# Optimization experiments

Measured on AMD Instinct MI355X. Metric: run time of the kernel, lower is better.

The kernel has to match this reference:

```python
import jax, jax.numpy as jnp
import numpy as np

B, C, H, W = 4, 256, 32, 32
DS, DC, EXP, NSL, NH = 16, 4, 2, 16, 2
DI = EXP * C
DTR = (C + 15) // 16


def layer_norm(x, w, b, eps=1e-5):
    m = x.mean(-1, keepdims=True)
    v = ((x - m) ** 2).mean(-1, keepdims=True)
    return (x - m) / jnp.sqrt(v + eps) * w + b


def conv2d(x, w, b, groups=1, pad=1):
    y = jax.lax.conv_general_dilated(x, w, (1, 1), [(pad, pad), (pad, pad)],
        dimension_numbers=('NCHW', 'OIHW', 'NCHW'), feature_group_count=groups)
    return y + b[None, :, None, None]


def causal_conv1d(x, w, b):
    k = w.shape[-1]
    y = jax.lax.conv_general_dilated(x, w, (1,), [(k - 1, 0)],
        dimension_numbers=('NCH', 'OIH', 'NCH'), feature_group_count=x.shape[1])
    return y + b[None, :, None]


def selective_scan(u, delta, A, Bm, Cm, D, z):
    # u, delta, z: (b,d,l); A: (d,n); Bm, Cm: (b,n,l); D: (d,)
    dA = jnp.exp(jnp.einsum('bdl,dn->lbdn', delta, A))
    dBu = jnp.einsum('bdl,bnl->lbdn', delta * u, Bm)
    Cl = jnp.moveaxis(Cm, -1, 0)  # (l,b,n)
    def step(s, inp):
        dA_t, dBu_t, C_t = inp
        s = dA_t * s + dBu_t
        return s, jnp.einsum('bdn,bn->bd', s, C_t)
    s0 = jnp.zeros(dA.shape[1:], dA.dtype)
    _, ys = jax.lax.scan(step, s0, (dA, dBu, Cl))
    y = jnp.moveaxis(ys, 0, -1) + D[None, :, None] * u
    return y * jax.nn.silu(z)


def mamba_inner(xz, cw, cb, xpw, dtw, dtb, A, D):
    d = xz.shape[1] // 2
    xm, z = xz[:, :d], xz[:, d:]
    xm = jax.nn.silu(causal_conv1d(xm, cw, cb))
    x_dbl = jnp.einsum('bdl,ed->ble', xm, xpw)  # e = dt_rank + 2*d_state
    dt = x_dbl[..., :DTR]
    Bm = x_dbl[..., DTR:DTR + DS]
    Cm = x_dbl[..., DTR + DS:]
    dt = jax.nn.softplus(jnp.einsum('blr,dr->bdl', dt, dtw) + dtb[None, :, None])
    return selective_scan(xm, dt, A, jnp.moveaxis(Bm, -1, 1), jnp.moveaxis(Cm, -1, 1), D, z)


def mamba_v3(hs, in_w, cw, cb, cbw, cbb, csw, csb, xpw, xpbw, xpsw,
             dtw, dtb, dtbw, dtbb, dtsw, dtsb, Alog, Ablog, Aslog, D, Db, Ds, outw):
    b, l, dm = hs.shape
    xz = jnp.einsum('bld,ed->bel', hs, in_w)  # (b, 2*DI, l)
    A, A_b, A_s = -jnp.exp(Alog), -jnp.exp(Ablog), -jnp.exp(Aslog)
    out = mamba_inner(xz, cw, cb, xpw, dtw, dtb, A, D)
    out_b = mamba_inner(xz[:, :, ::-1], cbw, cbb, xpbw, dtbw, dtbb, A_b, Db)
    # slice scan: torch.chunk(nslices,-1) -> stack(-1) -> flatten(-2)
    xz_s = xz.reshape(b, 2 * DI, NSL, l // NSL).transpose(0, 1, 3, 2).reshape(b, 2 * DI, l)
    out_s = mamba_inner(xz_s, csw, csb, xpsw, dtsw, dtsb, A_s, Ds)
    # restore: reshape(b,d,nslices,l//nslices).permute(0,1,3,2).flatten(-2)
    out_s = out_s.reshape(b, DI, NSL, l // NSL).transpose(0, 1, 3, 2).reshape(b, DI, l)
    comb = out + out_b[:, :, ::-1] + out_s
    return jnp.einsum('bdl,od->blo', comb, outw)


def forward(x, proj1_w, proj1_b, proj2_w, proj2_b, norm_w, norm_b,
            q_w, q_b, k_w, k_b, v_w, v_b, o_w, o_b, fc1_w, fc1_b, dw_w, dw_b,
            in_w, cw, cb, cbw, cbb, csw, csb, xpw, xpbw, xpsw,
            dtw, dtb, dtbw, dtbb, dtsw, dtsb, Alog, Ablog, Aslog, D, Db, Ds, outw):
    b, c, h, w = x.shape
    n = h * w
    x_skip = x
    # torch: x.transpose(1,2).reshape(B,C,H,W) -- memory reinterpret, replicated
    x_flat = jnp.transpose(x, (0, 2, 1, 3)).reshape(b, c, h, w)
    xc = conv2d(x_flat, proj1_w, proj1_b)
    xc = jnp.transpose(xc.reshape(b, c, n), (0, 2, 1))
    xc = layer_norm(xc, norm_w, norm_b)
    dh = c // NH
    Q = (xc @ q_w.T + q_b).reshape(b, n, NH, dh).transpose(0, 2, 1, 3)
    K = (xc @ k_w.T + k_b).reshape(b, n, NH, dh).transpose(0, 2, 1, 3)
    V = (xc @ v_w.T + v_b).reshape(b, n, NH, dh).transpose(0, 2, 1, 3)
    scores = jnp.einsum('bhqd,bhkd->bhqk', Q, K) / jnp.sqrt(jnp.float32(dh))
    probs = jax.nn.softmax(scores, axis=-1)
    att = jnp.einsum('bhqk,bhkd->bhqd', probs, V).transpose(0, 2, 1, 3).reshape(b, n, c)
    att = att @ o_w.T + o_b
    # torch: .view(B,C,HW).transpose(1,2) -- memory reinterpret, replicated
    x_att = jnp.transpose(att.reshape(b, c, n), (0, 2, 1))
    xm = mamba_v3(x_att, in_w, cw, cb, cbw, cbb, csw, csb, xpw, xpbw, xpsw,
                  dtw, dtb, dtbw, dtbb, dtsw, dtsb, Alog, Ablog, Aslog, D, Db, Ds, outw)
    xm = jnp.transpose(xm, (0, 2, 1)).reshape(b, c, h, w)
    xm = jax.nn.relu(conv2d(xm, proj1_w, proj1_b))  # proj1 reused (as in source)
    xm = jax.nn.relu(conv2d(xm, proj2_w, proj2_b, pad=0))
    xs = jnp.transpose(xm.reshape(b, c, n), (0, 2, 1))
    xf = xs @ fc1_w.T + fc1_b
    xd = jnp.transpose(xf, (0, 2, 1)).reshape(b, c, h, w)
    xd = conv2d(xd, dw_w, dw_b, groups=c)
    xd = jnp.transpose(xd.reshape(b, c, n), (0, 2, 1))
    out = jnp.transpose(xd.reshape(b, h, w, c), (0, 3, 1, 2)) + x_skip
    return out


def setup_inputs():
    keys = iter(jax.random.split(jax.random.key(0), 64))
    def rn(shape, s=0.02):
        return jax.random.normal(next(keys), shape, jnp.float32) * s
    Alog = jnp.log(jnp.tile(jnp.arange(1, DS + 1, dtype=jnp.float32), (DI, 1)))
    return dict(
        x=jax.random.normal(next(keys), (B, C, H, W), jnp.float32),
        proj1_w=rn((C, C, 3, 3)), proj1_b=jnp.zeros((C,), jnp.float32),
        proj2_w=rn((C, C, 1, 1)), proj2_b=jnp.zeros((C,), jnp.float32),
        norm_w=jnp.ones((C,), jnp.float32), norm_b=jnp.zeros((C,), jnp.float32),
        q_w=rn((C, C)), q_b=jnp.zeros((C,), jnp.float32),
        k_w=rn((C, C)), k_b=jnp.zeros((C,), jnp.float32),
        v_w=rn((C, C)), v_b=jnp.zeros((C,), jnp.float32),
        o_w=rn((C, C)), o_b=jnp.zeros((C,), jnp.float32),
        fc1_w=rn((C, C)), fc1_b=jnp.zeros((C,), jnp.float32),
        dw_w=rn((C, 1, 3, 3)), dw_b=jnp.zeros((C,), jnp.float32),
        in_w=rn((2 * DI, C)),
        cw=rn((DI, 1, DC), 0.1), cb=jnp.zeros((DI,), jnp.float32),
        cbw=rn((DI, 1, DC), 0.1), cbb=jnp.zeros((DI,), jnp.float32),
        csw=rn((DI, 1, DC), 0.1), csb=jnp.zeros((DI,), jnp.float32),
        xpw=rn((DTR + 2 * DS, DI)), xpbw=rn((DTR + 2 * DS, DI)), xpsw=rn((DTR + 2 * DS, DI)),
        dtw=rn((DI, DTR), 0.1), dtb=jnp.full((DI,), -4.6, jnp.float32),
        dtbw=rn((DI, DTR), 0.1), dtbb=jnp.full((DI,), -4.6, jnp.float32),
        dtsw=rn((DI, DTR), 0.1), dtsb=jnp.full((DI,), -4.6, jnp.float32),
        Alog=Alog, Ablog=Alog, Aslog=Alog,
        D=jnp.ones((DI,), jnp.float32), Db=jnp.ones((DI,), jnp.float32), Ds=jnp.ones((DI,), jnp.float32),
        outw=rn((C, DI)),
    )


def reference(x, proj1_w, proj1_b, proj2_w, proj2_b, norm_w, norm_b,
              q_w, q_b, k_w, k_b, v_w, v_b, o_w, o_b, fc1_w, fc1_b, dw_w, dw_b,
              in_w, cw, cb, cbw, cbb, csw, csb, xpw, xpbw, xpsw,
              dtw, dtb, dtbw, dtbb, dtsw, dtsb, Alog, Ablog, Aslog, D, Db, Ds, outw):
    return forward(x, proj1_w, proj1_b, proj2_w, proj2_b, norm_w, norm_b,
                   q_w, q_b, k_w, k_b, v_w, v_b, o_w, o_b, fc1_w, fc1_b, dw_w, dw_b,
                   in_w, cw, cb, cbw, cbb, csw, csb, xpw, xpbw, xpsw,
                   dtw, dtb, dtbw, dtbb, dtsw, dtsb, Alog, Ablog, Aslog, D, Db, Ds, outw)
```

## Files before the change

kernel.cpp:

```cpp
#include <hip/hip_runtime.h>


#define LOG2E 1.4426950408889634f
#define NCH 16
#define LCH 64

typedef unsigned short u16;
typedef unsigned int u32;
typedef __attribute__((ext_vector_type(8))) short bf16x8;
typedef __attribute__((ext_vector_type(4))) float f32x4;

__device__ __forceinline__ u16 f2b(float f) {
  u32 u = __builtin_bit_cast(u32, f);
  u32 r = (u + 0x7fffu + ((u >> 16) & 1u)) >> 16;
  return (u16)r;
}
__device__ __forceinline__ float b2f(u16 h) {
  u32 u = ((u32)h) << 16;
  return __builtin_bit_cast(float, u);
}

#define DPP_ADD(p, ctrl)                                                   \
  (p) += __builtin_bit_cast(float, __builtin_amdgcn_update_dpp(            \
             0, __builtin_bit_cast(int, (p)), ctrl, 0xF, 0xF, true))

static const long BRS = 44544;

struct BrP { const float *cw, *cb, *xpw, *dtw, *dtb, *Al, *Dv; };

__global__ __launch_bounds__(256) void pack_branch_k(float* __restrict__ dst0,
                                                     BrP p0, BrP p1, BrP p2) {
  int z = blockIdx.y;
  BrP p = (z == 0) ? p0 : ((z == 1) ? p1 : p2);
  float* dst = dst0 + (long)z * BRS;
  int t = blockIdx.x * 256 + threadIdx.x;
  if (t < 2048) dst[t] = p.cw[t];
  else if (t < 2560) dst[t] = p.cb[t - 2048];
  else if (t < 27136) dst[t] = p.xpw[t - 2560];
  else if (t < 35328) dst[t] = p.dtw[t - 27136];
  else if (t < 35840) dst[t] = p.dtb[t - 35328];
  else if (t < 44032) dst[t] = -expf(p.Al[t - 35840]) * LOG2E;
  else if (t < 44544) dst[t] = p.Dv[t - 44032];
}

__global__ __launch_bounds__(256) void pack_wb_k(
    const float* __restrict__ qw, const float* __restrict__ kw,
    const float* __restrict__ vw, const float* __restrict__ ow,
    const float* __restrict__ inw, const float* __restrict__ outw,
    const float* __restrict__ p2w, const float* __restrict__ fc1w,
    const float* __restrict__ qb, const float* __restrict__ kb,
    const float* __restrict__ vb, u16* __restrict__ WB,
    float* __restrict__ QBIAS) {
  int t = blockIdx.x * 256 + threadIdx.x;
  if (t < 65536) WB[t] = f2b(qw[t]);
  else if (t < 131072) WB[t] = f2b(kw[t - 65536]);
  else if (t < 196608) WB[t] = f2b(vw[t - 131072]);
  else if (t < 262144) WB[t] = f2b(ow[t - 196608]);
  else if (t < 524288) WB[t] = f2b(inw[t - 262144]);
  else if (t < 655360) WB[t] = f2b(outw[t - 524288]);
  else if (t < 720896) WB[t] = f2b(p2w[t - 655360]);
  else if (t < 786432) WB[t] = f2b(fc1w[t - 720896]);
  else if (t < 787200) {
    int i = t - 786432;
    QBIAS[i] = (i < 256) ? qb[i] : (i < 512 ? kb[i - 256] : vb[i - 512]);
  }
}

__global__ __launch_bounds__(256) void pack_wc_k(const float* __restrict__ w,
                                                 u16* __restrict__ wc) {
  int t = blockIdx.x * 256 + threadIdx.x;
  int ci = t & 255, khw = (t >> 8) % 9, co = t / 2304;
  wc[t] = f2b(w[co * 2304 + ci * 9 + khw]);
}

__global__ __launch_bounds__(256) void xin_k(const float* __restrict__ x,
                                             u16* __restrict__ xin) {
  int t = blockIdx.x * 256 + threadIdx.x;
  int ci = t & 255, w = (t >> 8) & 31, h = (t >> 13) & 31, b = t >> 18;
  int idx = ci * 32 + h;
  xin[t] = f2b(x[((long)b << 18) + ((long)(idx & 255) << 10) +
                 ((idx >> 8) << 5) + w]);
}

__global__ __launch_bounds__(256) void pack_wmb_k(const float* __restrict__ PB,
                                                  u16* __restrict__ WMB,
                                                  float* __restrict__ BIA) {
  int z = blockIdx.y;
  int t = blockIdx.x * 256 + threadIdx.x;
  const float* pb = PB + (long)z * BRS;
  if (t < 16384) {
    int r = t >> 9, k = t & 511;
    WMB[((long)z * 640 + r) * 512 + k] = f2b(pb[2560 + (16 + r) * 512 + k]);
  } else if (t < 65536) {
    int i = t - 16384;
    int r = 544 + (i >> 9), k = i & 511;
    WMB[((long)z * 640 + r) * 512 + k] = 0;
  } else if (t < 66176) {
    int i = t - 65536;
    float v = 0.f;
    if (i >= 32 && i < 544) v = pb[35328 + (i - 32)];
    BIA[(long)z * 640 + i] = v;
  }
}

__global__ __launch_bounds__(256) void pack_wdt_k(const float* __restrict__ PB,
                                                  u16* __restrict__ WMB) {
  int z = blockIdx.y, d = blockIdx.x;
  const float* pb = PB + (long)z * BRS;
  float dtwv[16];
  #pragma unroll
  for (int r = 0; r < 16; ++r) dtwv[r] = pb[27136 + d * 16 + r];
  #pragma unroll
  for (int i = 0; i < 2; ++i) {
    int k = threadIdx.x + i * 256;
    float acc = 0.f;
    #pragma unroll
    for (int r = 0; r < 16; ++r) acc = fmaf(dtwv[r], pb[2560 + r * 512 + k], acc);
    WMB[((long)z * 640 + 32 + d) * 512 + k] = f2b(acc);
  }
}

__global__ __launch_bounds__(256, 2) void conv_mfma_k(
    const u16* __restrict__ in, const u16* __restrict__ wc,
    const float* __restrict__ bias, float* __restrict__ outF,
    u16* __restrict__ outH, int relu) {
  __shared__ u16 ldsA[4][64][8];
  __shared__ u16 ldsB[4][64][8];
  int m0 = blockIdx.x * 64, n0 = blockIdx.y * 64;
  int tid = threadIdx.x;
  int lane = tid & 63, wv = tid >> 6;
  int row = tid & 63, k8 = tid >> 6;
  int l = m0 + row;
  int h = (l >> 5) & 31, w = l & 31;
  int rlo = lane & 15, khl = lane >> 4;
  f32x4 acc[4];
  #pragma unroll
  for (int n = 0; n < 4; ++n) acc[n] = (f32x4){0.f, 0.f, 0.f, 0.f};
  for (int t = 0; t < 72; ++t) {
    int kh = t / 24, r = t % 24, kw = r >> 3, ci0 = (r & 7) << 5;
    __syncthreads();
    bf16x8 av = (bf16x8){0, 0, 0, 0, 0, 0, 0, 0};
    int hh = h + kh - 1, ww = w + kw - 1;
    if ((unsigned)hh < 32u && (unsigned)ww < 32u)
      av = *(const bf16x8*)&in[(long)(l + (kh - 1) * 32 + (kw - 1)) * 256 +
                               ci0 + k8 * 8];
    *(bf16x8*)&ldsA[k8][row][0] = av;
    *(bf16x8*)&ldsB[k8][row][0] =
        *(const bf16x8*)&wc[(long)(n0 + row) * 2304 + t * 32 + k8 * 8];
    __syncthreads();
    bf16x8 af = *(const bf16x8*)&ldsA[khl][wv * 16 + rlo][0];
    #pragma unroll
    for (int n = 0; n < 4; ++n) {
      bf16x8 bf = *(const bf16x8*)&ldsB[khl][n * 16 + rlo][0];
      acc[n] = __builtin_amdgcn_mfma_f32_16x16x32_bf16(af, bf, acc[n], 0, 0, 0);
    }
  }
  int rowb = (lane >> 4) * 4;
  #pragma unroll
  for (int n = 0; n < 4; ++n) {
    int gn = n0 + n * 16 + rlo;
    float bv = bias[gn];
    #pragma unroll
    for (int j = 0; j < 4; ++j) {
      int gm = m0 + wv * 16 + rowb + j;
      float v = acc[n][j] + bv;
      if (relu) v = fmaxf(v, 0.f);
      long oi = (long)gm * 256 + gn;
      if (outH) outH[oi] = f2b(v);
      else outF[oi] = v;
    }
  }
}

__global__ __launch_bounds__(256) void layernorm_k(const float* __restrict__ x,
                                                   const float* __restrict__ w,
                                                   const float* __restrict__ b,
                                                   u16* __restrict__ o) {
  int row = blockIdx.x * 4 + (threadIdx.x >> 6);
  int lane = threadIdx.x & 63;
  float4 v = ((const float4*)(x + (long)row * 256))[lane];
  float s = v.x + v.y + v.z + v.w;
  #pragma unroll
  for (int m = 32; m; m >>= 1) s += __shfl_xor(s, m);
  float mean = s * (1.f / 256.f);
  float4 dv = {v.x - mean, v.y - mean, v.z - mean, v.w - mean};
  float vs = dv.x * dv.x + dv.y * dv.y + dv.z * dv.z + dv.w * dv.w;
  #pragma unroll
  for (int m = 32; m; m >>= 1) vs += __shfl_xor(vs, m);
  float inv = rsqrtf(vs * (1.f / 256.f) + 1e-5f);
  float4 wv = ((const float4*)w)[lane];
  float4 bv = ((const float4*)b)[lane];
  u32 lo = (u32)f2b(dv.x * inv * wv.x + bv.x) |
           ((u32)f2b(dv.y * inv * wv.y + bv.y) << 16);
  u32 hi = (u32)f2b(dv.z * inv * wv.z + bv.z) |
           ((u32)f2b(dv.w * inv * wv.w + bv.w) << 16);
  ((uint2*)(o + (long)row * 256))[lane] = make_uint2(lo, hi);
}

__global__ __launch_bounds__(256) void softmax_k(const float* __restrict__ S,
                                                 u16* __restrict__ P) {
  int row = blockIdx.x * 4 + (threadIdx.x >> 6);
  int lane = threadIdx.x & 63;
  const float4* p = (const float4*)(S + (long)row * 1024);
  float4 v[4];
  float m = -1e30f;
  #pragma unroll
  for (int i = 0; i < 4; ++i) {
    v[i] = p[lane * 4 + i];
    m = fmaxf(m, fmaxf(fmaxf(v[i].x, v[i].y), fmaxf(v[i].z, v[i].w)));
  }
  #pragma unroll
  for (int q = 32; q; q >>= 1) m = fmaxf(m, __shfl_xor(m, q));
  float s = 0.f;
  #pragma unroll
  for (int i = 0; i < 4; ++i) {
    v[i].x = expf(v[i].x - m); v[i].y = expf(v[i].y - m);
    v[i].z = expf(v[i].z - m); v[i].w = expf(v[i].w - m);
    s += v[i].x + v[i].y + v[i].z + v[i].w;
  }
  #pragma unroll
  for (int q = 32; q; q >>= 1) s += __shfl_xor(s, q);
  float inv = 1.f / s;
  uint2* q2 = (uint2*)(P + (long)row * 1024);
  #pragma unroll
  for (int i = 0; i < 4; ++i) {
    u32 lo = (u32)f2b(v[i].x * inv) | ((u32)f2b(v[i].y * inv) << 16);
    u32 hi = (u32)f2b(v[i].z * inv) | ((u32)f2b(v[i].w * inv) << 16);
    q2[lane * 4 + i] = make_uint2(lo, hi);
  }
}

__global__ __launch_bounds__(256, 2) void bgemm_k(
    const u16* __restrict__ A, const u16* __restrict__ B,
    const float* __restrict__ bias, float* __restrict__ OutF,
    u16* __restrict__ OutH, int M, int N, int K,
    int lda, int ldb, int ldo, int zdiv,
    long a_zb, long a_zh, long b_zb, long b_zh, long o_zb, long o_zh,
    float alpha, int act, int bias_zb, float* __restrict__ Out2,
    const float* __restrict__ Aux) {
  __shared__ u16 ldsA[4][128][8];
  __shared__ u16 ldsB[4][128][8];
  int z = blockIdx.z, zb = z / zdiv, zh = z - zb * zdiv;
  const u16* Ab = A + zb * a_zb + zh * a_zh;
  const u16* Bb = B + zb * b_zb + zh * b_zh;
  const float* biasb = bias ? bias + (long)zb * bias_zb : nullptr;
  long ob = zb * o_zb + zh * o_zh;
  int m0 = blockIdx.x * 128, n0 = blockIdx.y * 128;
  int tid = threadIdx.x;
  int lane = tid & 63, wv = tid >> 6;
  int wr = wv >> 1, wc = wv & 1;
  int r1 = tid & 127, h1 = tid >> 7;
  int r2 = r1, h2 = h1 + 2;
  const u16* a1 = Ab + (long)(m0 + r1) * lda + h1 * 8;
  const u16* a2 = Ab + (long)(m0 + r2) * lda + h2 * 8;
  const u16* b1 = Bb + (long)(n0 + r1) * ldb + h1 * 8;
  const u16* b2 = Bb + (long)(n0 + r2) * ldb + h2 * 8;

  f32x4 acc[4][4];
  #pragma unroll
  for (int i = 0; i < 4; ++i)
    #pragma unroll
    for (int j = 0; j < 4; ++j) acc[i][j] = (f32x4){0.f, 0.f, 0.f, 0.f};

  bf16x8 ra1 = *(const bf16x8*)a1;
  bf16x8 ra2 = *(const bf16x8*)a2;
  bf16x8 rb1 = *(const bf16x8*)b1;
  bf16x8 rb2 = *(const bf16x8*)b2;

  int nt = K >> 5;
  int kh = lane >> 4, rlo = lane & 15;
  for (int t = 0; t < nt; ++t) {
    __syncthreads();
    *(bf16x8*)&ldsA[h1][r1][0] = ra1;
    *(bf16x8*)&ldsA[h2][r2][0] = ra2;
    *(bf16x8*)&ldsB[h1][r1][0] = rb1;
    *(bf16x8*)&ldsB[h2][r2][0] = rb2;
    if (t + 1 < nt) {
      int ko = (t + 1) << 5;
      ra1 = *(const bf16x8*)(a1 + ko);
      ra2 = *(const bf16x8*)(a2 + ko);
      rb1 = *(const bf16x8*)(b1 + ko);
      rb2 = *(const bf16x8*)(b2 + ko);
    }
    __syncthreads();
    bf16x8 af[4], bfr[4];
    #pragma unroll
    for (int m = 0; m < 4; ++m)
      af[m] = *(const bf16x8*)&ldsA[kh][wr * 64 + m * 16 + rlo][0];
    #pragma unroll
    for (int n = 0; n < 4; ++n)
      bfr[n] = *(const bf16x8*)&ldsB[kh][wc * 64 + n * 16 + rlo][0];
    #pragma unroll
    for (int m = 0; m < 4; ++m)
      #pragma unroll
      for (int n = 0; n < 4; ++n)
        acc[m][n] = __builtin_amdgcn_mfma_f32_16x16x32_bf16(af[m], bfr[n],
                                                            acc[m][n], 0, 0, 0);
  }
  int rowb = (lane >> 4) * 4;
  #pragma unroll
  for (int m = 0; m < 4; ++m) {
    #pragma unroll
    for (int n = 0; n < 4; ++n) {
      int gn = n0 + wc * 64 + n * 16 + rlo;
      float bv = biasb ? biasb[gn] : 0.f;
      #pragma unroll
      for (int j = 0; j < 4; ++j) {
        int gm = m0 + wr * 64 + m * 16 + rowb + j;
        float v = acc[m][n][j] * alpha + bv;
        if (act == 4) {
          if (gn < 32) {
            Out2[(long)(zb * 4096 + gm) * 32 + gn] = v;
          } else if (gn < 544) {
            float sp = (v > 30.f) ? v : log1pf(expf(v));
            long di = (long)(zb * 4096 + gm) * 512 + (gn - 32);
            ((float2*)OutF)[di] = make_float2(sp, Aux[di]);
          }
        } else {
          if (act == 1) v = fmaxf(v, 0.f);
          long oi = ob + (long)gm * ldo + gn;
          if (OutH) OutH[oi] = f2b(v);
          else OutF[oi] = v;
        }
      }
    }
  }
}

__global__ __launch_bounds__(256) void vt_k(const u16* __restrict__ qkv,
                                            u16* __restrict__ vt) {
  int t = blockIdx.x * 256 + threadIdx.x;
  int j = t & 1023, d = (t >> 10) & 127, bh = t >> 17;
  int b = bh >> 1, h = bh & 1;
  vt[t] = qkv[((long)(b * 1024 + j)) * 768 + 512 + h * 128 + d];
}

__global__ __launch_bounds__(256) void xatt_k(const float* __restrict__ hs,
                                              u16* __restrict__ xa) {
  int t = blockIdx.x * 256 + threadIdx.x;
  int dm = t & 255, l = (t >> 8) & 1023, b = t >> 18;
  xa[t] = f2b(hs[((long)b << 18) + dm * 1024 + l]);
}

__device__ __forceinline__ int brmap(int br, int j) {
  if (br == 0) return j;
  if (br == 1) return 1023 - j;
  return ((j & 15) << 6) | (j >> 4);
}

__global__ __launch_bounds__(256) void cconv_k(const u16* __restrict__ xzb,
                                               const float* __restrict__ pk,
                                               float* __restrict__ xmc,
                                               u16* __restrict__ xmcb,
                                               u16* __restrict__ zs) {
  long t = (long)blockIdx.x * 256 + threadIdx.x;
  int d = (int)(t & 511);
  long r = t >> 9;
  int j = (int)(r & 1023);
  int bb = (int)(r >> 10);
  int b = bb & 3, br = bb >> 2;
  const float* pb = pk + (long)br * BRS;
  float acc = pb[2048 + d];
  #pragma unroll
  for (int tap = 0; tap < 4; ++tap) {
    int jj = j - 3 + tap;
    if (jj >= 0) {
      int l = brmap(br, jj);
      acc = fmaf(b2f(xzb[(((long)b << 10) + l) * 1024 + d]), pb[d * 4 + tap],
                 acc);
    }
  }
  float sig = 1.f / (1.f + expf(-acc));
  float u = acc * sig;
  xmc[t] = u;
  xmcb[t] = f2b(u);
  int l = brmap(br, j);
  float zv = b2f(xzb[(((long)b << 10) + l) * 1024 + 512 + d]);
  zs[t] = f2b(zv / (1.f + expf(-zv)));
}

__global__ __launch_bounds__(256) void scanA_k(
    const float2* __restrict__ du, const float* __restrict__ xdbl,
    const float* __restrict__ pk, float* __restrict__ SE,
    float* __restrict__ PC) {
  __shared__ float bs[LCH][16];
  int tid = threadIdx.x;
  int wv = tid >> 6, lane = tid & 63;
  int q = lane & 3, dl = lane >> 2;
  int bb = blockIdx.x >> 3, dch = blockIdx.x & 7;
  int br = bb >> 2, b = bb & 3;
  int d = dch * 64 + wv * 16 + dl;
  int c = blockIdx.y;
  long xdb = (long)br * 131072 + (long)b * 32768 + (long)(c * LCH) * 32;
  {
    int j = tid >> 2, g = tid & 3;
    *(float4*)&bs[j][g * 4] = *(const float4*)&xdbl[xdb + j * 32 + g * 4];
  }
  __syncthreads();
  const float* pb = pk + (long)br * BRS;
  float4 Aln = *(const float4*)&pb[35840 + d * 16 + q * 4];
  long obase = ((long)bb << 19) + (long)(c * LCH) * 512 + d;
  const float2* pdu = du + obase;
  float4 s = {0.f, 0.f, 0.f, 0.f};
  float S = 0.f;
  #pragma unroll 4
  for (int jl = 0; jl < LCH; ++jl) {
    float2 dv = pdu[(long)jl * 512];
    float w = dv.x * dv.y;
    float4 Bv = *(const float4*)&bs[jl][q * 4];
    s.x = fmaf(exp2f(dv.x * Aln.x), s.x, w * Bv.x);
    s.y = fmaf(exp2f(dv.x * Aln.y), s.y, w * Bv.y);
    s.z = fmaf(exp2f(dv.x * Aln.z), s.z, w * Bv.z);
    s.w = fmaf(exp2f(dv.x * Aln.w), s.w, w * Bv.w);
    S += dv.x;
  }
  long si = ((((long)bb) * NCH + c) * 512 + d) * 16 + q * 4;
  *(float4*)&SE[si] = s;
  float4 P = {exp2f(Aln.x * S), exp2f(Aln.y * S),
              exp2f(Aln.z * S), exp2f(Aln.w * S)};
  *(float4*)&PC[si] = P;
}

__global__ __launch_bounds__(256) void scanB_k(const float* __restrict__ SE,
                                               const float* __restrict__ PC,
                                               float* __restrict__ SI) {
  long t = (long)blockIdx.x * 256 + threadIdx.x;
  int n = (int)(t & 15);
  int d = (int)((t >> 4) & 511);
  int bb = (int)(t >> 13);
  float run = 0.f;
  for (int c = 0; c < NCH; ++c) {
    long si = (((long)bb * NCH + c) * 512 + d) * 16 + n;
    SI[si] = run;
    run = fmaf(PC[si], run, SE[si]);
  }
}

__global__ __launch_bounds__(256) void scanC_k(
    const float2* __restrict__ du, const float* __restrict__ xdbl,
    const u16* __restrict__ zs, const float* __restrict__ pk,
    const float* __restrict__ SI, u16* __restrict__ y) {
  __shared__ float bcs[LCH][32];
  int tid = threadIdx.x;
  int wv = tid >> 6, lane = tid & 63;
  int q = lane & 3, dl = lane >> 2;
  int bb = blockIdx.x >> 3, dch = blockIdx.x & 7;
  int br = bb >> 2, b = bb & 3;
  int d = dch * 64 + wv * 16 + dl;
  int c = blockIdx.y;
  long xdb = (long)br * 131072 + (long)b * 32768 + (long)(c * LCH) * 32;
  #pragma unroll
  for (int i = 0; i < 2; ++i) {
    int idx = tid + i * 256;
    int j = idx >> 3, g = idx & 7;
    *(float4*)&bcs[j][g * 4] = *(const float4*)&xdbl[xdb + j * 32 + g * 4];
  }
  __syncthreads();
  const float* pb = pk + (long)br * BRS;
  float4 Aln = *(const float4*)&pb[35840 + d * 16 + q * 4];
  float Dv = pb[44032 + d];
  long obase = ((long)bb << 19) + (long)(c * LCH) * 512 + d;
  long si = ((((long)bb) * NCH + c) * 512 + d) * 16 + q * 4;
  float4 s = *(const float4*)&SI[si];
  const float2* pdu = du + obase;
  const u16* pzs = zs + obase;
  u16* py = y + obase;
  #pragma unroll 4
  for (int jl = 0; jl < LCH; ++jl) {
    float2 dv = pdu[(long)jl * 512];
    float w = dv.x * dv.y;
    float4 Bv = *(const float4*)&bcs[jl][q * 4];
    float4 Cv = *(const float4*)&bcs[jl][16 + q * 4];
    s.x = fmaf(exp2f(dv.x * Aln.x), s.x, w * Bv.x);
    s.y = fmaf(exp2f(dv.x * Aln.y), s.y, w * Bv.y);
    s.z = fmaf(exp2f(dv.x * Aln.z), s.z, w * Bv.z);
    s.w = fmaf(exp2f(dv.x * Aln.w), s.w, w * Bv.w);
    float p = s.x * Cv.x;
    p = fmaf(s.y, Cv.y, p);
    p = fmaf(s.z, Cv.z, p);
    p = fmaf(s.w, Cv.w, p);
    DPP_ADD(p, 0xB1);
    DPP_ADD(p, 0x4E);
    if (q == 0)
      py[(long)jl * 512] = f2b((p + Dv * dv.y) * b2f(pzs[(long)jl * 512]));
  }
}

__global__ __launch_bounds__(256) void combine_k(const u16* __restrict__ y,
                                                 u16* __restrict__ comb) {
  long t = (long)blockIdx.x * 256 + threadIdx.x;
  int d = (int)(t & 511);
  long r = t >> 9;
  int l = (int)(r & 1023);
  int b = (int)(r >> 10);
  int j2 = ((l & 63) << 4) | (l >> 6);
  float v = b2f(y[(((long)b << 10) + l) * 512 + d])
          + b2f(y[(((long)(4 + b) << 10) + (1023 - l)) * 512 + d])
          + b2f(y[(((long)(8 + b) << 10) + j2) * 512 + d]);
  comb[t] = f2b(v);
}

__global__ __launch_bounds__(256) void dw_k(const u16* __restrict__ xfb,
                                            const float* __restrict__ dww,
                                            const float* __restrict__ dwb,
                                            const float* __restrict__ x,
                                            float* __restrict__ out) {
  __shared__ float plane[1024];
  int bc = blockIdx.x;
  int b = bc >> 8, c = bc & 255;
  int tid = threadIdx.x;
  #pragma unroll
  for (int i = 0; i < 4; ++i) {
    int n = tid + i * 256;
    plane[n] = b2f(xfb[(((long)b << 10) + n) * 256 + c]);
  }
  __syncthreads();
  float wv[9];
  #pragma unroll
  for (int k = 0; k < 9; ++k) wv[k] = dww[c * 9 + k];
  float bb = dwb[c];
  long obase = ((long)(b * 256 + c)) << 10;
  #pragma unroll
  for (int i = 0; i < 4; ++i) {
    int n = tid + i * 256;
    int h = n >> 5, w = n & 31;
    float acc = bb;
    #pragma unroll
    for (int kh = 0; kh < 3; ++kh) {
      int hh = h + kh - 1;
      if ((unsigned)hh >= 32u) continue;
      #pragma unroll
      for (int kw = 0; kw < 3; ++kw) {
        int ww = w + kw - 1;
        if ((unsigned)ww >= 32u) continue;
        acc = fmaf(plane[hh * 32 + ww], wv[kh * 3 + kw], acc);
      }
    }
    out[obase + n] = acc + x[obase + n];
  }
}

extern "C" void kernel_launch(void* const* d_in, const int* in_sizes, int n_in,
                              void* d_out, int out_size, void* d_ws, size_t ws_size,
                              hipStream_t stream) {
  (void)in_sizes; (void)n_in; (void)out_size; (void)ws_size;
  const float* x    = (const float*)d_in[0];
  const float* p1w  = (const float*)d_in[1];
  const float* p1b  = (const float*)d_in[2];
  const float* p2w  = (const float*)d_in[3];
  const float* p2b  = (const float*)d_in[4];
  const float* nw   = (const float*)d_in[5];
  const float* nb   = (const float*)d_in[6];
  const float* qw   = (const float*)d_in[7];
  const float* qb   = (const float*)d_in[8];
  const float* kw   = (const float*)d_in[9];
  const float* kb   = (const float*)d_in[10];
  const float* vw   = (const float*)d_in[11];
  const float* vb   = (const float*)d_in[12];
  const float* ow   = (const float*)d_in[13];
  const float* ob   = (const float*)d_in[14];
  const float* fc1w = (const float*)d_in[15];
  const float* fc1b = (const float*)d_in[16];
  const float* dww  = (const float*)d_in[17];
  const float* dwb  = (const float*)d_in[18];
  const float* inw  = (const float*)d_in[19];
  const float* cw   = (const float*)d_in[20];
  const float* cb   = (const float*)d_in[21];
  const float* cbw  = (const float*)d_in[22];
  const float* cbb  = (const float*)d_in[23];
  const float* csw  = (const float*)d_in[24];
  const float* csb  = (const float*)d_in[25];
  const float* xpw  = (const float*)d_in[26];
  const float* xpbw = (const float*)d_in[27];
  const float* xpsw = (const float*)d_in[28];
  const float* dtw  = (const float*)d_in[29];
  const float* dtb  = (const float*)d_in[30];
  const float* dtbw = (const float*)d_in[31];
  const float* dtbb = (const float*)d_in[32];
  const float* dtsw = (const float*)d_in[33];
  const float* dtsb = (const float*)d_in[34];
  const float* Alog = (const float*)d_in[35];
  const float* Ablog= (const float*)d_in[36];
  const float* Aslog= (const float*)d_in[37];
  const float* Dv   = (const float*)d_in[38];
  const float* Dbv  = (const float*)d_in[39];
  const float* Dsv  = (const float*)d_in[40];
  const float* outw = (const float*)d_in[41];
  float* out = (float*)d_out;

  float* ws    = (float*)d_ws;
  float* PB    = ws;
  u16*   WCONV = (u16*)(ws + 140000);
  u16*   WB    = (u16*)(ws + 440000);
  float* QBIAS = ws + 840000;
  u16*   XINB  = (u16*)(ws + 850000);
  float* R     = ws + 1400000;

  u16*    XZB  = (u16*)R;
  float2* DU   = (float2*)R;
  u16*    ZS   = (u16*)(R + 12600000);
  float*  XMC  = R + 15750000;
  float*  SE   = R + 15750000;
  float*  PC   = R + 17350000;
  float*  SI   = R + 19000000;
  u16*    Y    = (u16*)(R + 20600000);
  u16*    XMCB = (u16*)(R + 22050000);
  u16*   COMBB = (u16*)(R + 23750000);
  float*  XDBL = R + 25200000;
  u16*    WMB  = (u16*)(R + 25600000);
  float*  BIA  = R + 26100000;
  float* XCT   = R + 4300000;
  u16*   XCTB  = (u16*)(R + 5400000);
  u16*   QKVB  = (u16*)(R + 6000000);
  u16*   VT    = (u16*)(R + 7600000);
  float* SC    = R + 8200000;
  u16*   P     = (u16*)(R + 16600000);
  u16*   ATTB  = (u16*)(R + 20900000);
  float* HS    = R + 21500000;
  u16*   XATTB = (u16*)(R + 22600000);
  u16*   XMBB  = (u16*)R;
  u16*   XM2B  = (u16*)(R + 600000);
  u16*   XPB   = (u16*)(R + 1200000);
  u16*   XFB   = (u16*)(R + 1800000);

  u16* WQKVB = WB;
  u16* OWB   = WB + 196608;
  u16* INWB  = WB + 262144;
  u16* OUTWB = WB + 524288;
  u16* P2WB  = WB + 655360;
  u16* FC1WB = WB + 720896;

  auto bgemm = [&](const u16* A, const u16* Bm, const float* bias,
                   float* OutF, u16* OutH, int M, int N, int K,
                   int lda, int ldb, int ldo, int nz, int zdiv,
                   long a_zb, long a_zh, long b_zb, long b_zh,
                   long o_zb, long o_zh, float alpha, int act,
                   int bias_zb, float* Out2, const float* Aux) {
    dim3 g(M / 128, N / 128, nz);
    bgemm_k<<<g, 256, 0, stream>>>(A, Bm, bias, OutF, OutH, M, N, K,
                                   lda, ldb, ldo, zdiv, a_zb, a_zh,
                                   b_zb, b_zh, o_zb, o_zh, alpha, act,
                                   bias_zb, Out2, Aux);
  };

  BrP b0 = {cw, cb, xpw, dtw, dtb, Alog, Dv};
  BrP b1 = {cbw, cbb, xpbw, dtbw, dtbb, Ablog, Dbv};
  BrP b2 = {csw, csb, xpsw, dtsw, dtsb, Aslog, Dsv};
  pack_branch_k<<<dim3(174, 3), 256, 0, stream>>>(PB, b0, b1, b2);
  pack_wb_k<<<3075, 256, 0, stream>>>(qw, kw, vw, ow, inw, outw, p2w, fc1w,
                                      qb, kb, vb, WB, QBIAS);
  pack_wc_k<<<2304, 256, 0, stream>>>(p1w, WCONV);
  xin_k<<<4096, 256, 0, stream>>>(x, XINB);
  pack_wmb_k<<<dim3(259, 3), 256, 0, stream>>>(PB, WMB, BIA);
  pack_wdt_k<<<dim3(512, 3), 256, 0, stream>>>(PB, WMB);

  conv_mfma_k<<<dim3(64, 4), 256, 0, stream>>>(XINB, WCONV, p1b, XCT, nullptr, 0);
  layernorm_k<<<1024, 256, 0, stream>>>(XCT, nw, nb, XCTB);

  bgemm(XCTB, WQKVB, QBIAS, nullptr, QKVB, 4096, 768, 256, 256, 256, 768,
        1, 1, 0, 0, 0, 0, 0, 0, 1.f, 0, 0, nullptr, nullptr);
  vt_k<<<4096, 256, 0, stream>>>(QKVB, VT);

  bgemm(QKVB, QKVB + 256, nullptr, SC, nullptr, 1024, 1024, 128, 768, 768, 1024,
        8, 2, 786432, 128, 786432, 128, 2097152, 1048576,
        0.08838834764831845f, 0, 0, nullptr, nullptr);
  softmax_k<<<2048, 256, 0, stream>>>(SC, P);

  bgemm(P, VT, nullptr, nullptr, ATTB, 1024, 128, 1024, 1024, 1024, 256,
        8, 2, 2097152, 1048576, 262144, 131072, 262144, 128, 1.f, 0,
        0, nullptr, nullptr);

  bgemm(ATTB, OWB, ob, HS, nullptr, 4096, 256, 256, 256, 256, 256,
        1, 1, 0, 0, 0, 0, 0, 0, 1.f, 0, 0, nullptr, nullptr);
  xatt_k<<<4096, 256, 0, stream>>>(HS, XATTB);

  bgemm(XATTB, INWB, nullptr, nullptr, XZB, 1024, 1024, 256, 256, 256, 1024,
        4, 1, 262144, 0, 0, 0, 1048576, 0, 1.f, 0, 0, nullptr, nullptr);

  cconv_k<<<24576, 256, 0, stream>>>(XZB, PB, XMC, XMCB, ZS);

  bgemm(XMCB, WMB, BIA, (float*)DU, nullptr, 4096, 640, 512, 512, 512, 0,
        3, 1, 2097152, 0, 327680, 0, 0, 0, 1.f, 4, 640, XDBL, XMC);

  scanA_k<<<dim3(96, NCH), 256, 0, stream>>>(DU, XDBL, PB, SE, PC);
  scanB_k<<<384, 256, 0, stream>>>(SE, PC, SI);
  scanC_k<<<dim3(96, NCH), 256, 0, stream>>>(DU, XDBL, ZS, PB, SI, Y);

  combine_k<<<8192, 256, 0, stream>>>(Y, COMBB);

  bgemm(COMBB, OUTWB, nullptr, nullptr, XMBB, 4096, 256, 512, 512, 512, 256,
        1, 1, 0, 0, 0, 0, 0, 0, 1.f, 0, 0, nullptr, nullptr);

  conv_mfma_k<<<dim3(64, 4), 256, 0, stream>>>(XMBB, WCONV, p1b, nullptr, XM2B, 1);

  bgemm(XM2B, P2WB, p2b, nullptr, XPB, 4096, 256, 256, 256, 256, 256,
        1, 1, 0, 0, 0, 0, 0, 0, 1.f, 1, 0, nullptr, nullptr);

  bgemm(XPB, FC1WB, fc1b, nullptr, XFB, 4096, 256, 256, 256, 256, 256,
        1, 1, 0, 0, 0, 0, 0, 0, 1.f, 0, 0, nullptr, nullptr);

  dw_k<<<1024, 256, 0, stream>>>(XFB, dww, dwb, x, out);
}
```

Measured before the change: 672.0 us.

## Pack delta/u as bf16 pairs and add 64x64 GEMM tile kernel

The x_proj GEMM epilogue now writes softplus(delta) and the conv output u as a packed bf16 pair in one 32-bit word instead of a float2, and the scan kernels unpack it. The fp32 copy of the conv output is dropped from cconv_k. This halves the traffic on the largest intermediate. A new 64x64-tile bgemm kernel is used for the small-N GEMMs (P@V, out-proj, mamba out, proj2, fc1) to launch more blocks and improve occupancy. The cost is reduced precision of delta and u in the scan.

```diff
diff --git a/kernel.cpp b/kernel.cpp
--- a/kernel.cpp
+++ b/kernel.cpp
@@ -237,7 +237,7 @@
     int lda, int ldb, int ldo, int zdiv,
     long a_zb, long a_zh, long b_zb, long b_zh, long o_zb, long o_zh,
     float alpha, int act, int bias_zb, float* __restrict__ Out2,
-    const float* __restrict__ Aux) {
+    const u16* __restrict__ Aux) {
   __shared__ u16 ldsA[4][128][8];
   __shared__ u16 ldsB[4][128][8];
   int z = blockIdx.z, zb = z / zdiv, zh = z - zb * zdiv;
@@ -314,7 +314,7 @@
           } else if (gn < 544) {
             float sp = (v > 30.f) ? v : log1pf(expf(v));
             long di = (long)(zb * 4096 + gm) * 512 + (gn - 32);
-            ((float2*)OutF)[di] = make_float2(sp, Aux[di]);
+            ((u32*)OutF)[di] = (u32)f2b(sp) | ((u32)Aux[di] << 16);
           }
         } else {
           if (act == 1) v = fmaxf(v, 0.f);
@@ -327,6 +327,66 @@
   }
 }
 
+__global__ __launch_bounds__(256, 2) void bgemm64_k(
+    const u16* __restrict__ A, const u16* __restrict__ B,
+    const float* __restrict__ bias, float* __restrict__ OutF,
+    u16* __restrict__ OutH, int M, int N, int K,
+    int lda, int ldb, int ldo, int zdiv,
+    long a_zb, long a_zh, long b_zb, long b_zh, long o_zb, long o_zh,
+    float alpha, int act) {
+  __shared__ u16 ldsA[4][64][8];
+  __shared__ u16 ldsB[4][64][8];
+  int z = blockIdx.z, zb = z / zdiv, zh = z - zb * zdiv;
+  const u16* Ab = A + zb * a_zb + zh * a_zh;
+  const u16* Bb = B + zb * b_zb + zh * b_zh;
+  long ob = zb * o_zb + zh * o_zh;
+  int m0 = blockIdx.x * 64, n0 = blockIdx.y * 64;
+  int tid = threadIdx.x;
+  int lane = tid & 63, wv = tid >> 6;
+  int row = tid & 63, k8 = tid >> 6;
+  int rlo = lane & 15, khl = lane >> 4;
+  const u16* pa = Ab + (long)(m0 + row) * lda + k8 * 8;
+  const u16* pb = Bb + (long)(n0 + row) * ldb + k8 * 8;
+  f32x4 acc[4];
+  #pragma unroll
+  for (int n = 0; n < 4; ++n) acc[n] = (f32x4){0.f, 0.f, 0.f, 0.f};
+  bf16x8 ra = *(const bf16x8*)pa;
+  bf16x8 rb = *(const bf16x8*)pb;
+  int nt = K >> 5;
+  for (int t = 0; t < nt; ++t) {
+    __syncthreads();
+    *(bf16x8*)&ldsA[k8][row][0] = ra;
+    *(bf16x8*)&ldsB[k8][row][0] = rb;
+    if (t + 1 < nt) {
+      int ko = (t + 1) << 5;
+      ra = *(const bf16x8*)(pa + ko);
+      rb = *(const bf16x8*)(pb + ko);
+    }
+    __syncthreads();
+    bf16x8 af = *(const bf16x8*)&ldsA[khl][wv * 16 + rlo][0];
+    #pragma unroll
+    for (int n = 0; n < 4; ++n) {
+      bf16x8 bf = *(const bf16x8*)&ldsB[khl][n * 16 + rlo][0];
+      acc[n] = __builtin_amdgcn_mfma_f32_16x16x32_bf16(af, bf, acc[n], 0, 0, 0);
+    }
+  }
+  int rowb = (lane >> 4) * 4;
+  #pragma unroll
+  for (int n = 0; n < 4; ++n) {
+    int gn = n0 + n * 16 + rlo;
+    float bv = bias ? bias[gn] : 0.f;
+    #pragma unroll
+    for (int j = 0; j < 4; ++j) {
+      int gm = m0 + wv * 16 + rowb + j;
+      float v = acc[n][j] * alpha + bv;
+      if (act == 1) v = fmaxf(v, 0.f);
+      long oi = ob + (long)gm * ldo + gn;
+      if (OutH) OutH[oi] = f2b(v);
+      else OutF[oi] = v;
+    }
+  }
+}
+
 __global__ __launch_bounds__(256) void vt_k(const u16* __restrict__ qkv,
                                             u16* __restrict__ vt) {
   int t = blockIdx.x * 256 + threadIdx.x;
@@ -350,7 +410,6 @@
 
 __global__ __launch_bounds__(256) void cconv_k(const u16* __restrict__ xzb,
                                                const float* __restrict__ pk,
-                                               float* __restrict__ xmc,
                                                u16* __restrict__ xmcb,
                                                u16* __restrict__ zs) {
   long t = (long)blockIdx.x * 256 + threadIdx.x;
@@ -371,16 +430,14 @@
     }
   }
   float sig = 1.f / (1.f + expf(-acc));
-  float u = acc * sig;
-  xmc[t] = u;
-  xmcb[t] = f2b(u);
+  xmcb[t] = f2b(acc * sig);
   int l = brmap(br, j);
   float zv = b2f(xzb[(((long)b << 10) + l) * 1024 + 512 + d]);
   zs[t] = f2b(zv / (1.f + expf(-zv)));
 }
 
 __global__ __launch_bounds__(256) void scanA_k(
-    const float2* __restrict__ du, const float* __restrict__ xdbl,
+    const u32* __restrict__ du, const float* __restrict__ xdbl,
     const float* __restrict__ pk, float* __restrict__ SE,
     float* __restrict__ PC) {
   __shared__ float bs[LCH][16];
@@ -400,19 +457,21 @@
   const float* pb = pk + (long)br * BRS;
   float4 Aln = *(const float4*)&pb[35840 + d * 16 + q * 4];
   long obase = ((long)bb << 19) + (long)(c * LCH) * 512 + d;
-  const float2* pdu = du + obase;
+  const u32* pdu = du + obase;
   float4 s = {0.f, 0.f, 0.f, 0.f};
   float S = 0.f;
   #pragma unroll 4
   for (int jl = 0; jl < LCH; ++jl) {
-    float2 dv = pdu[(long)jl * 512];
-    float w = dv.x * dv.y;
+    u32 dv = pdu[(long)jl * 512];
+    float delta = b2f((u16)dv);
+    float uu = b2f((u16)(dv >> 16));
+    float w = delta * uu;
     float4 Bv = *(const float4*)&bs[jl][q * 4];
-    s.x = fmaf(exp2f(dv.x * Aln.x), s.x, w * Bv.x);
-    s.y = fmaf(exp2f(dv.x * Aln.y), s.y, w * Bv.y);
-    s.z = fmaf(exp2f(dv.x * Aln.z), s.z, w * Bv.z);
-    s.w = fmaf(exp2f(dv.x * Aln.w), s.w, w * Bv.w);
-    S += dv.x;
+    s.x = fmaf(exp2f(delta * Aln.x), s.x, w * Bv.x);
+    s.y = fmaf(exp2f(delta * Aln.y), s.y, w * Bv.y);
+    s.z = fmaf(exp2f(delta * Aln.z), s.z, w * Bv.z);
+    s.w = fmaf(exp2f(delta * Aln.w), s.w, w * Bv.w);
+    S += delta;
   }
   long si = ((((long)bb) * NCH + c) * 512 + d) * 16 + q * 4;
   *(float4*)&SE[si] = s;
@@ -437,7 +496,7 @@
 }
 
 __global__ __launch_bounds__(256) void scanC_k(
-    const float2* __restrict__ du, const float* __restrict__ xdbl,
+    const u32* __restrict__ du, const float* __restrict__ xdbl,
     const u16* __restrict__ zs, const float* __restrict__ pk,
     const float* __restrict__ SI, u16* __restrict__ y) {
   __shared__ float bcs[LCH][32];
@@ -462,19 +521,21 @@
   long obase = ((long)bb << 19) + (long)(c * LCH) * 512 + d;
   long si = ((((long)bb) * NCH + c) * 512 + d) * 16 + q * 4;
   float4 s = *(const float4*)&SI[si];
-  const float2* pdu = du + obase;
+  const u32* pdu = du + obase;
   const u16* pzs = zs + obase;
   u16* py = y + obase;
   #pragma unroll 4
   for (int jl = 0; jl < LCH; ++jl) {
-    float2 dv = pdu[(long)jl * 512];
-    float w = dv.x * dv.y;
+    u32 dv = pdu[(long)jl * 512];
+    float delta = b2f((u16)dv);
+    float uu = b2f((u16)(dv >> 16));
+    float w = delta * uu;
     float4 Bv = *(const float4*)&bcs[jl][q * 4];
     float4 Cv = *(const float4*)&bcs[jl][16 + q * 4];
-    s.x = fmaf(exp2f(dv.x * Aln.x), s.x, w * Bv.x);
-    s.y = fmaf(exp2f(dv.x * Aln.y), s.y, w * Bv.y);
-    s.z = fmaf(exp2f(dv.x * Aln.z), s.z, w * Bv.z);
-    s.w = fmaf(exp2f(dv.x * Aln.w), s.w, w * Bv.w);
+    s.x = fmaf(exp2f(delta * Aln.x), s.x, w * Bv.x);
+    s.y = fmaf(exp2f(delta * Aln.y), s.y, w * Bv.y);
+    s.z = fmaf(exp2f(delta * Aln.z), s.z, w * Bv.z);
+    s.w = fmaf(exp2f(delta * Aln.w), s.w, w * Bv.w);
     float p = s.x * Cv.x;
     p = fmaf(s.y, Cv.y, p);
     p = fmaf(s.z, Cv.z, p);
@@ -482,7 +543,7 @@
     DPP_ADD(p, 0xB1);
     DPP_ADD(p, 0x4E);
     if (q == 0)
-      py[(long)jl * 512] = f2b((p + Dv * dv.y) * b2f(pzs[(long)jl * 512]));
+      py[(long)jl * 512] = f2b((p + Dv * uu) * b2f(pzs[(long)jl * 512]));
   }
 }
 
@@ -597,13 +658,12 @@
   float* R     = ws + 1400000;
 
   u16*    XZB  = (u16*)R;
-  float2* DU   = (float2*)R;
+  u32*    DUB  = (u32*)R;
+  u16*    Y    = (u16*)(R + 6400000);
   u16*    ZS   = (u16*)(R + 12600000);
-  float*  XMC  = R + 15750000;
   float*  SE   = R + 15750000;
   float*  PC   = R + 17350000;
   float*  SI   = R + 19000000;
-  u16*    Y    = (u16*)(R + 20600000);
   u16*    XMCB = (u16*)(R + 22050000);
   u16*   COMBB = (u16*)(R + 23750000);
   float*  XDBL = R + 25200000;
@@ -635,12 +695,22 @@
                    int lda, int ldb, int ldo, int nz, int zdiv,
                    long a_zb, long a_zh, long b_zb, long b_zh,
                    long o_zb, long o_zh, float alpha, int act,
-                   int bias_zb, float* Out2, const float* Aux) {
+                   int bias_zb, float* Out2, const u16* Aux) {
     dim3 g(M / 128, N / 128, nz);
     bgemm_k<<<g, 256, 0, stream>>>(A, Bm, bias, OutF, OutH, M, N, K,
                                    lda, ldb, ldo, zdiv, a_zb, a_zh,
                                    b_zb, b_zh, o_zb, o_zh, alpha, act,
                                    bias_zb, Out2, Aux);
+  };
+  auto bgemm64 = [&](const u16* A, const u16* Bm, const float* bias,
+                     float* OutF, u16* OutH, int M, int N, int K,
+                     int lda, int ldb, int ldo, int nz, int zdiv,
+                     long a_zb, long a_zh, long b_zb, long b_zh,
+                     long o_zb, long o_zh, float alpha, int act) {
+    dim3 g(M / 64, N / 64, nz);
+    bgemm64_k<<<g, 256, 0, stream>>>(A, Bm, bias, OutF, OutH, M, N, K,
+                                     lda, ldb, ldo, zdiv, a_zb, a_zh,
+                                     b_zb, b_zh, o_zb, o_zh, alpha, act);
   };
 
   BrP b0 = {cw, cb, xpw, dtw, dtb, Alog, Dv};
@@ -666,38 +736,37 @@
         0.08838834764831845f, 0, 0, nullptr, nullptr);
   softmax_k<<<2048, 256, 0, stream>>>(SC, P);
 
-  bgemm(P, VT, nullptr, nullptr, ATTB, 1024, 128, 1024, 1024, 1024, 256,
-        8, 2, 2097152, 1048576, 262144, 131072, 262144, 128, 1.f, 0,
-        0, nullptr, nullptr);
-
-  bgemm(ATTB, OWB, ob, HS, nullptr, 4096, 256, 256, 256, 256, 256,
-        1, 1, 0, 0, 0, 0, 0, 0, 1.f, 0, 0, nullptr, nullptr);
+  bgemm64(P, VT, nullptr, nullptr, ATTB, 1024, 128, 1024, 1024, 1024, 256,
+          8, 2, 2097152, 1048576, 262144, 131072, 262144, 128, 1.f, 0);
+
+  bgemm64(ATTB, OWB, ob, HS, nullptr, 4096, 256, 256, 256, 256, 256,
+          1, 1, 0, 0, 0, 0, 0, 0, 1.f, 0);
   xatt_k<<<4096, 256, 0, stream>>>(HS, XATTB);
 
   bgemm(XATTB, INWB, nullptr, nullptr, XZB, 1024, 1024, 256, 256, 256, 1024,
         4, 1, 262144, 0, 0, 0, 1048576, 0, 1.f, 0, 0, nullptr, nullptr);
 
-  cconv_k<<<24576, 256, 0, stream>>>(XZB, PB, XMC, XMCB, ZS);
-
-  bgemm(XMCB, WMB, BIA, (float*)DU, nullptr, 4096, 640, 512, 512, 512, 0,
-        3, 1, 2097152, 0, 327680, 0, 0, 0, 1.f, 4, 640, XDBL, XMC);
-
-  scanA_k<<<dim3(96, NCH), 256, 0, stream>>>(DU, XDBL, PB, SE, PC);
+  cconv_k<<<24576, 256, 0, stream>>>(XZB, PB, XMCB, ZS);
+
+  bgemm(XMCB, WMB, BIA, (float*)DUB, nullptr, 4096, 640, 512, 512, 512, 0,
+        3, 1, 2097152, 0, 327680, 0, 0, 0, 1.f, 4, 640, XDBL, XMCB);
+
+  scanA_k<<<dim3(96, NCH), 256, 0, stream>>>(DUB, XDBL, PB, SE, PC);
   scanB_k<<<384, 256, 0, stream>>>(SE, PC, SI);
-  scanC_k<<<dim3(96, NCH), 256, 0, stream>>>(DU, XDBL, ZS, PB, SI, Y);
+  scanC_k<<<dim3(96, NCH), 256, 0, stream>>>(DUB, XDBL, ZS, PB, SI, Y);
 
   combine_k<<<8192, 256, 0, stream>>>(Y, COMBB);
 
-  bgemm(COMBB, OUTWB, nullptr, nullptr, XMBB, 4096, 256, 512, 512, 512, 256,
-        1, 1, 0, 0, 0, 0, 0, 0, 1.f, 0, 0, nullptr, nullptr);
+  bgemm64(COMBB, OUTWB, nullptr, nullptr, XMBB, 4096, 256, 512, 512, 512, 256,
+          1, 1, 0, 0, 0, 0, 0, 0, 1.f, 0);
 
   conv_mfma_k<<<dim3(64, 4), 256, 0, stream>>>(XMBB, WCONV, p1b, nullptr, XM2B, 1);
 
-  bgemm(XM2B, P2WB, p2b, nullptr, XPB, 4096, 256, 256, 256, 256, 256,
-        1, 1, 0, 0, 0, 0, 0, 0, 1.f, 1, 0, nullptr, nullptr);
-
-  bgemm(XPB, FC1WB, fc1b, nullptr, XFB, 4096, 256, 256, 256, 256, 256,
-        1, 1, 0, 0, 0, 0, 0, 0, 1.f, 0, 0, nullptr, nullptr);
+  bgemm64(XM2B, P2WB, p2b, nullptr, XPB, 4096, 256, 256, 256, 256, 256,
+          1, 1, 0, 0, 0, 0, 0, 0, 1.f, 1);
+
+  bgemm64(XPB, FC1WB, fc1b, nullptr, XFB, 4096, 256, 256, 256, 256, 256,
+          1, 1, 0, 0, 0, 0, 0, 0, 1.f, 0);
 
   dw_k<<<1024, 256, 0, stream>>>(XFB, dww, dwb, x, out);
 }
```

Measured after the change: 597.8 us. 11.0% less time.
